# Performance work log

Measured on AMD Instinct MI355X. Metric: run time of the kernel, lower is better.

The kernel has to match this reference:

```python
import jax, jax.numpy as jnp
import numpy as np

T = 0.07        # temperature (hardcoded in CCM)
BN_EPS = 1e-5   # torch BatchNorm1d default eps (eval mode, running stats)


def _l2norm(x):
    # torch F.normalize(dim=1): x / max(||x||, 1e-12)
    n = jnp.linalg.norm(x, axis=1, keepdims=True)
    return x / jnp.maximum(n, 1e-12)


def _attn(q, k):
    # cosine similarity scaled by 1/t and 1/sqrt(num_keys)
    scale = jnp.asarray(k.shape[0], q.dtype) ** 0.5
    return (_l2norm(q) @ _l2norm(k).T) / T / scale


def setup_inputs() -> dict:
    key = jax.random.key(0)
    ks = jax.random.split(key, 24)
    D, N, BS, C, H = 2048, 1024, 64, 65, 128
    f32 = jnp.float32
    def g(k, shape, scale=1.0):
        return jax.random.normal(k, shape, f32) * scale
    return {
        "all_f": g(ks[0], (BS, D)),
        "embedding": _l2norm(g(ks[1], (N, D))),  # memory queue (normalized at init)
        "all_y": jax.random.randint(ks[2], (BS,), 0, C),
        "head_w1": g(ks[3], (D, H), 1.0 / np.sqrt(D)),
        "head_b1": jnp.zeros((H,), f32),
        "head_g": jax.random.uniform(ks[4], (H,), f32) + 0.5,
        "head_beta": g(ks[5], (H,), 0.1),
        "head_rm": g(ks[6], (H,), 0.1),
        "head_rv": jax.random.uniform(ks[7], (H,), f32) + 0.5,
        "head_w2": g(ks[8], (H, H), 1.0 / np.sqrt(H)),
        "head_b2": jnp.zeros((H,), f32),
        "mix_w1": g(ks[9], (2 * H, H), 1.0 / np.sqrt(2 * H)),
        "mix_b1": jnp.zeros((H,), f32),
        "mix_g": jax.random.uniform(ks[10], (H,), f32) + 0.5,
        "mix_beta": g(ks[11], (H,), 0.1),
        "mix_rm": g(ks[12], (H,), 0.1),
        "mix_rv": jax.random.uniform(ks[13], (H,), f32) + 0.5,
        "mix_w2": g(ks[14], (H, D), 1.0 / np.sqrt(H)),
        "mix_b2": jnp.zeros((D,), f32),
        "clf_w": g(ks[15], (D, C), 1.0 / np.sqrt(D)),
        "clf_b": jnp.zeros((C,), f32),
    }


def reference(all_f, embedding, all_y,
              head_w1, head_b1, head_g, head_beta, head_rm, head_rv, head_w2, head_b2,
              mix_w1, mix_b1, mix_g, mix_beta, mix_rm, mix_rv, mix_w2, mix_b2,
              clf_w, clf_b):
    # CCM.causal(all_f, embedding, all_y): returns [bs, num_classes]
    H = head_b2.shape[0]
    # z|x attention over the memory queue
    z_x = jax.nn.softmax(_attn(all_f, embedding), axis=-1)          # [bs, N]

    def head(x):
        h = x @ head_w1 + head_b1
        h = (h - head_rm) * jax.lax.rsqrt(head_rv + BN_EPS) * head_g + head_beta
        return jax.nn.relu(h) @ head_w2 + head_b2                   # [., 128]

    hf = head(all_f)        # [bs, 128]
    hz = head(embedding)    # [N, 128]
    # mixer layer 1 on concat([hf, hz]) decomposed into two matmuls + broadcast add
    h1 = hf @ mix_w1[:H] + mix_b1                                   # [bs, 128]
    h1 = h1[:, None, :] + (hz @ mix_w1[H:])[None, :, :]             # [bs, N, 128]
    h1 = (h1 - mix_rm) * jax.lax.rsqrt(mix_rv + BN_EPS) * mix_g + mix_beta
    h1 = jax.nn.relu(h1)
    mixed = h1 @ mix_w2 + mix_b2                                    # [bs, N, D]
    y_zx = jax.nn.softmax(mixed @ clf_w + clf_b, axis=-1)           # [bs, N, C] = p(y|z,x)
    # p(x): self-attention row-sums, softmax over the batch (all_y given -> this branch)
    p_x = jax.nn.softmax(_attn(all_f, all_f).sum(axis=1), axis=0)   # [bs]
    sum_x = jnp.einsum('b,bnc->nc', p_x, y_zx)                      # [N, C]
    return z_x @ sum_x                                              # [bs, C]
```

## Files before the change

### kernel.cpp

```cpp
#include <hip/hip_runtime.h>
#include <hip/hip_bf16.h>
#include <math.h>

#define D   2048
#define NQ  1024
#define BSZ 64
#define NC  65
#define HD  128

#define OFF_SCALEH 0
#define OFF_CH     128
#define OFF_BZC    256
#define OFF_BAC    384
#define OFF_BVEC   512
#define OFF_PXP    640
#define OFF_WC     896
#define OFF_A2T    6016
#define OFF_B2     14208
#define OFF_SP     145280
#define OFF_SUMX   669568
#define OFF_FNB    751488
#define OFF_AFB    817024
#define OFF_EMBB   882560
#define OFF_W1T    1931136
#define OFF_WZT    2062208
#define OFF_WAT    2070400
#define OFF_MW2B   2078592
#define OFF_CWT    2226048

typedef __attribute__((ext_vector_type(8))) short    bf16x8;
typedef __attribute__((ext_vector_type(4))) float    f32x4;
typedef __attribute__((ext_vector_type(8))) unsigned short u16x8;
typedef __attribute__((ext_vector_type(2))) unsigned short u16x2;

__device__ inline unsigned short f2b(float v) {
    __hip_bfloat16 h = __float2bfloat16(v);
    return __builtin_bit_cast(unsigned short, h);
}

__global__ void __launch_bounds__(256) k_prep(const float* __restrict__ all_f,
                                              const float* __restrict__ emb,
                                              const float* __restrict__ head_w1,
                                              const float* __restrict__ head_b1,
                                              const float* __restrict__ head_g,
                                              const float* __restrict__ head_beta,
                                              const float* __restrict__ head_rm,
                                              const float* __restrict__ head_rv,
                                              const float* __restrict__ head_w2,
                                              const float* __restrict__ head_b2,
                                              const float* __restrict__ mix_w1,
                                              const float* __restrict__ mix_b1,
                                              const float* __restrict__ mix_g,
                                              const float* __restrict__ mix_beta,
                                              const float* __restrict__ mix_rm,
                                              const float* __restrict__ mix_rv,
                                              const float* __restrict__ mix_w2,
                                              const float* __restrict__ mix_b2,
                                              const float* __restrict__ clf_w,
                                              float* __restrict__ ws) {
    __shared__ float sbuf[128*66];
    int bid = blockIdx.x, t = threadIdx.x;
    if (bid == 0) {
        int h = t & 127, jq = t >> 7;
        float sb = 0.f, sa = 0.f;
        #pragma unroll 8
        for (int j = jq*64; j < jq*64 + 64; ++j) {
            float b2v = head_b2[j];
            sb = fmaf(b2v, mix_w1[(HD + j)*HD + h], sb);
            sa = fmaf(b2v, mix_w1[j*HD + h], sa);
        }
        sbuf[jq*256 + h]       = sb;
        sbuf[jq*256 + 128 + h] = sa;
        __syncthreads();
        if (jq == 0) {
            float s = head_g[h] * rsqrtf(head_rv[h] + 1e-5f);
            ws[OFF_SCALEH + h] = s;
            ws[OFF_CH + h] = (head_b1[h] - head_rm[h]) * s + head_beta[h];
            float ms = mix_g[h] * rsqrtf(mix_rv[h] + 1e-5f);
            float msh = mix_beta[h] - mix_rm[h] * ms;
            float sbT = sbuf[h] + sbuf[256 + h];
            float saT = sbuf[128 + h] + sbuf[256 + 128 + h];
            ws[OFF_BZC + h] = sbT * ms;
            ws[OFF_BAC + h] = fmaf(saT + mix_b1[h], ms, msh);
        }
    } else if (bid < 129) {
        int j = bid - 1;
        int h = t & 127, which = t >> 7;
        const float* M1 = mix_w1 + (which ? 0 : HD*HD);
        float ms = mix_g[h] * rsqrtf(mix_rv[h] + 1e-5f);
        float acc = 0.f;
        #pragma unroll 8
        for (int k = 0; k < HD; ++k)
            acc = fmaf(head_w2[j*HD + k], M1[k*HD + h], acc);
        unsigned short* dst = (unsigned short*)(ws + (which ? OFF_WAT : OFF_WZT));
        dst[h*HD + j] = f2b(acc * ms);
    } else if (bid < 147) {
        int r0 = (bid - 129) * 8;
        unsigned short* dst = (unsigned short*)(ws + OFF_MW2B);
        int i0 = t * 8;
        for (int rr = 0; rr < 8; ++rr) {
            int r = r0 + rr;
            u16x8 o;
            if (r < HD || r == HD) {
                const float* src = (r < HD) ? (mix_w2 + (size_t)r * D) : mix_b2;
                float4 f1 = *(const float4*)(src + i0);
                float4 f2 = *(const float4*)(src + i0 + 4);
                o[0]=f2b(f1.x); o[1]=f2b(f1.y); o[2]=f2b(f1.z); o[3]=f2b(f1.w);
                o[4]=f2b(f2.x); o[5]=f2b(f2.y); o[6]=f2b(f2.z); o[7]=f2b(f2.w);
            } else {
                o[0]=0;o[1]=0;o[2]=0;o[3]=0;o[4]=0;o[5]=0;o[6]=0;o[7]=0;
            }
            *(u16x8*)(dst + (size_t)r*D + i0) = o;
        }
    } else if (bid < 163) {
        int k0 = (bid - 147) * 128;
        float (*tile)[66] = (float(*)[66])sbuf;
        for (int i = t; i < 128*65; i += 256) {
            int r = i / 65;
            tile[r][i - 65*r] = clf_w[(size_t)k0*65 + i];
        }
        __syncthreads();
        unsigned short* cwt = (unsigned short*)(ws + OFF_CWT);
        for (int idx = t; idx < 80*16; idx += 256) {
            int c = idx >> 4, kq = idx & 15;
            u16x8 v;
            #pragma unroll
            for (int j = 0; j < 8; ++j)
                v[j] = (c < NC) ? f2b(tile[kq*8 + j][c]) : (unsigned short)0;
            *(u16x8*)(cwt + (size_t)c*D + k0 + kq*8) = v;
        }
    } else if (bid < 227) {
        int b = bid - 163;
        const float* src = all_f + (size_t)b * D;
        int i0 = t * 8;
        float4 f1 = *(const float4*)(src + i0);
        float4 f2 = *(const float4*)(src + i0 + 4);
        float s = f1.x*f1.x + f1.y*f1.y + f1.z*f1.z + f1.w*f1.w
                + f2.x*f2.x + f2.y*f2.y + f2.z*f2.z + f2.w*f2.w;
        sbuf[t] = s; __syncthreads();
        for (int k = 128; k > 0; k >>= 1) { if (t < k) sbuf[t] += sbuf[t + k]; __syncthreads(); }
        float rn = 1.f / fmaxf(sqrtf(sbuf[0]), 1e-12f);
        unsigned short* fnb = (unsigned short*)(ws + OFF_FNB) + (size_t)b * D;
        unsigned short* afb = (unsigned short*)(ws + OFF_AFB) + (size_t)b * D;
        u16x8 on, oa;
        on[0]=f2b(f1.x*rn); on[1]=f2b(f1.y*rn); on[2]=f2b(f1.z*rn); on[3]=f2b(f1.w*rn);
        on[4]=f2b(f2.x*rn); on[5]=f2b(f2.y*rn); on[6]=f2b(f2.z*rn); on[7]=f2b(f2.w*rn);
        oa[0]=f2b(f1.x); oa[1]=f2b(f1.y); oa[2]=f2b(f1.z); oa[3]=f2b(f1.w);
        oa[4]=f2b(f2.x); oa[5]=f2b(f2.y); oa[6]=f2b(f2.z); oa[7]=f2b(f2.w);
        *(u16x8*)(fnb + i0) = on;
        *(u16x8*)(afb + i0) = oa;
    } else if (bid < 483) {
        int n0 = (bid - 227) * 4;
        unsigned short* dst = (unsigned short*)(ws + OFF_EMBB);
        int i0 = t * 8;
        for (int r = 0; r < 4; ++r) {
            const float* src = emb + (size_t)(n0 + r) * D;
            float4 f1 = *(const float4*)(src + i0);
            float4 f2 = *(const float4*)(src + i0 + 4);
            u16x8 o;
            o[0]=f2b(f1.x); o[1]=f2b(f1.y); o[2]=f2b(f1.z); o[3]=f2b(f1.w);
            o[4]=f2b(f2.x); o[5]=f2b(f2.y); o[6]=f2b(f2.z); o[7]=f2b(f2.w);
            *(u16x8*)(dst + (size_t)(n0 + r)*D + i0) = o;
        }
    } else {
        int rb = bid - 483;
        float (*tile)[33] = (float(*)[33])sbuf;
        int k0 = (rb >> 2) * 128, h0 = (rb & 3) * 32;
        int hh = t & 31, kk = t >> 5;
        for (int r = 0; r < 16; ++r)
            tile[kk + r*8][hh] = head_w1[(size_t)(k0 + kk + r*8)*HD + h0 + hh];
        __syncthreads();
        unsigned short* dst = (unsigned short*)(ws + OFF_W1T);
        int kcol = (t & 63) * 2, hrow = t >> 6;
        for (int r = 0; r < 8; ++r) {
            int h = hrow + r*4;
            u16x2 v;
            v[0] = f2b(tile[kcol][h]);
            v[1] = f2b(tile[kcol + 1][h]);
            *(u16x2*)(dst + (size_t)(h0 + h)*D + k0 + kcol) = v;
        }
    }
}

__global__ void __launch_bounds__(512) k_main(const float* __restrict__ clf_b,
                                              float* __restrict__ ws) {
    __shared__ float part[2][32][128];
    __shared__ unsigned short ush[32][136];
    __shared__ float wcp[8][16][16];
    int bid = blockIdx.x, t = threadIdx.x;
    int lane = t & 63, wv = t >> 6;
    int row16 = lane & 15, kgrp = lane >> 4;
    if (bid < 128) {
        const unsigned short* fnb  = (const unsigned short*)(ws + OFF_FNB);
        const unsigned short* embb = (const unsigned short*)(ws + OFF_EMBB);
        int nt = bid & 15, ks = bid >> 4;
        int b0 = (wv & 3) * 16;
        int n0 = nt*64 + (wv >> 2) * 32;
        const unsigned short* Ap = fnb  + (size_t)(b0 + row16)*D + ks*256 + kgrp*8;
        const unsigned short* B0 = embb + (size_t)(n0 + row16)*D + ks*256 + kgrp*8;
        const unsigned short* B1 = B0 + 16*D;
        f32x4 a0 = {0,0,0,0}, a1 = {0,0,0,0};
        #pragma unroll
        for (int s = 0; s < 8; ++s) {
            bf16x8 a = *(const bf16x8*)(Ap + s*32);
            a0 = __builtin_amdgcn_mfma_f32_16x16x32_bf16(a, *(const bf16x8*)(B0 + s*32), a0, 0, 0, 0);
            a1 = __builtin_amdgcn_mfma_f32_16x16x32_bf16(a, *(const bf16x8*)(B1 + s*32), a1, 0, 0, 0);
        }
        float* Sp = ws + OFF_SP + (size_t)ks * BSZ * NQ;
        #pragma unroll
        for (int r = 0; r < 4; ++r) {
            float* rowp = Sp + (size_t)(b0 + kgrp*4 + r)*NQ + n0;
            rowp[row16]      = a0[r];
            rowp[16 + row16] = a1[r];
        }
    } else if (bid < 162) {
        int tile = bid - 128;
        bool isF = tile >= 32;
        const unsigned short* Arow = isF
            ? (const unsigned short*)(ws + OFF_AFB) + (size_t)(tile - 32) * 32 * D
            : (const unsigned short*)(ws + OFF_EMBB) + (size_t)tile * 32 * D;
        const unsigned short* w1t = (const unsigned short*)(ws + OFF_W1T);
        int hgrp = wv & 3, kh = wv >> 2;
        const unsigned short* Ap = Arow + (size_t)row16*D + kh*1024 + kgrp*8;
        const unsigned short* B0 = w1t + (size_t)(hgrp*32 + row16)*D + kh*1024 + kgrp*8;
        const unsigned short* B1 = B0 + 16*D;
        f32x4 h00 = {0,0,0,0}, h01 = {0,0,0,0}, h10 = {0,0,0,0}, h11 = {0,0,0,0};
        #pragma unroll 4
        for (int s = 0; s < 32; ++s) {
            bf16x8 a0 = *(const bf16x8*)(Ap + s*32);
            bf16x8 a1 = *(const bf16x8*)(Ap + 16*D + s*32);
            bf16x8 b0 = *(const bf16x8*)(B0 + s*32);
            bf16x8 b1 = *(const bf16x8*)(B1 + s*32);
            h00 = __builtin_amdgcn_mfma_f32_16x16x32_bf16(a0, b0, h00, 0, 0, 0);
            h01 = __builtin_amdgcn_mfma_f32_16x16x32_bf16(a0, b1, h01, 0, 0, 0);
            h10 = __builtin_amdgcn_mfma_f32_16x16x32_bf16(a1, b0, h10, 0, 0, 0);
            h11 = __builtin_amdgcn_mfma_f32_16x16x32_bf16(a1, b1, h11, 0, 0, 0);
        }
        int mb = kgrp*4, hc0 = hgrp*32 + row16, hc1 = hc0 + 16;
        #pragma unroll
        for (int r = 0; r < 4; ++r) {
            part[kh][mb + r][hc0]      = h00[r];
            part[kh][mb + r][hc1]      = h01[r];
            part[kh][16 + mb + r][hc0] = h10[r];
            part[kh][16 + mb + r][hc1] = h11[r];
        }
        __syncthreads();
        {
            int row = t >> 4, cg = (t & 15) * 8;
            #pragma unroll
            for (int j = 0; j < 8; ++j) {
                int col = cg + j;
                float v = part[0][row][col] + part[1][row][col];
                ush[row][col] = f2b(fmaxf(fmaf(v, ws[OFF_SCALEH + col], ws[OFF_CH + col]), 0.f));
            }
        }
        __syncthreads();
        {
            int rt = wv >> 2, wv2 = wv & 3;
            const unsigned short* wt = (const unsigned short*)(ws + (isF ? OFF_WAT : OFF_WZT));
            const unsigned short* W0 = wt + (size_t)(wv2*32 + row16)*HD + kgrp*8;
            const unsigned short* W1b = W0 + 16*HD;
            f32x4 o0 = {0,0,0,0}, o1 = {0,0,0,0};
            #pragma unroll
            for (int s = 0; s < 4; ++s) {
                bf16x8 a = *(const bf16x8*)(&ush[rt*16 + row16][s*32 + kgrp*8]);
                o0 = __builtin_amdgcn_mfma_f32_16x16x32_bf16(a, *(const bf16x8*)(W0 + s*32), o0, 0, 0, 0);
                o1 = __builtin_amdgcn_mfma_f32_16x16x32_bf16(a, *(const bf16x8*)(W1b + s*32), o1, 0, 0, 0);
            }
            int hcA = wv2*32 + row16, hcB = hcA + 16;
            int boff = isF ? OFF_BAC : OFF_BZC;
            float bz0 = ws[boff + hcA], bz1 = ws[boff + hcB];
            float* outp = isF ? (ws + OFF_A2T + (size_t)(tile - 32)*32*HD)
                              : (ws + OFF_B2  + (size_t)tile*32*HD);
            #pragma unroll
            for (int r = 0; r < 4; ++r) {
                outp[(size_t)(rt*16 + mb + r)*HD + hcA] = o0[r] + bz0;
                outp[(size_t)(rt*16 + mb + r)*HD + hcB] = o1[r] + bz1;
            }
        }
    } else if (bid < 207) {
        int w = bid - 162;
        int mt = w / 5, ntile = w % 5;
        const unsigned short* mw2b = (const unsigned short*)(ws + OFF_MW2B);
        const unsigned short* cwt  = (const unsigned short*)(ws + OFF_CWT);
        const unsigned short* Ap = mw2b + (size_t)(mt*16 + row16)*D + wv*256 + kgrp*8;
        const unsigned short* Bp = cwt  + (size_t)(ntile*16 + row16)*D + wv*256 + kgrp*8;
        f32x4 acc = {0,0,0,0};
        #pragma unroll
        for (int s = 0; s < 8; ++s)
            acc = __builtin_amdgcn_mfma_f32_16x16x32_bf16(
                *(const bf16x8*)(Ap + s*32), *(const bf16x8*)(Bp + s*32), acc, 0, 0, 0);
        #pragma unroll
        for (int r = 0; r < 4; ++r)
            wcp[wv][kgrp*4 + r][row16] = acc[r];
        __syncthreads();
        if (t < 256) {
            int j = t >> 4, c16 = t & 15;
            float s = 0.f;
            #pragma unroll
            for (int q = 0; q < 8; ++q) s += wcp[q][j][c16];
            int jj = mt*16 + j, c = ntile*16 + c16;
            unsigned short* wct = (unsigned short*)(ws + OFF_WC);
            if (jj < HD)       wct[(size_t)c*HD + jj] = f2b(s);
            else if (jj == HD) ws[OFF_BVEC + c] = (c < NC) ? s + clf_b[c] : -1e30f;
        }
    } else {
        int pb = bid - 207;
        const unsigned short* fnb = (const unsigned short*)(ws + OFF_FNB);
        int bq = wv & 3, kq = (wv >> 2) + pb*2;
        int b0 = bq*16;
        const unsigned short* Ap = fnb + (size_t)(b0 + row16)*D + kq*512 + kgrp*8;
        const unsigned short* Bp = fnb + (size_t)row16*D + kq*512 + kgrp*8;
        f32x4 acc[4];
        #pragma unroll
        for (int nt = 0; nt < 4; ++nt) acc[nt] = (f32x4){0.f,0.f,0.f,0.f};
        #pragma unroll 2
        for (int s = 0; s < 16; ++s) {
            bf16x8 a = *(const bf16x8*)(Ap + s*32);
            #pragma unroll
            for (int nt = 0; nt < 4; ++nt)
                acc[nt] = __builtin_amdgcn_mfma_f32_16x16x32_bf16(
                    a, *(const bf16x8*)(Bp + (size_t)nt*16*D + s*32), acc[nt], 0, 0, 0);
        }
        #pragma unroll
        for (int r = 0; r < 4; ++r) {
            float v = acc[0][r] + acc[1][r] + acc[2][r] + acc[3][r];
            v += __shfl_xor(v, 1); v += __shfl_xor(v, 2);
            v += __shfl_xor(v, 4); v += __shfl_xor(v, 8);
            if (row16 == 0)
                ws[OFF_PXP + kq*64 + b0 + kgrp*4 + r] = v;
        }
    }
}

__global__ void __launch_bounds__(256) k_mix_mfma(float* __restrict__ ws) {
    __shared__ unsigned short wcs[80][136];
    __shared__ float redp[4][80];
    int t = threadIdx.x, lane = t & 63, wv = t >> 6;
    int n = blockIdx.x;
    int row16 = lane & 15, kgrp = lane >> 4;
    const unsigned short* wct = (const unsigned short*)(ws + OFF_WC);
    for (int i = t; i < 80*16; i += 256) {
        int r = i >> 4, cc = (i & 15) * 8;
        *(u16x8*)&wcs[r][cc] = *(const u16x8*)(wct + (size_t)r*HD + cc);
    }
    const float invTS = 1.0f / (0.07f * 8.0f);
    float sv = (ws[OFF_PXP + lane] + ws[OFF_PXP + 64 + lane]
              + ws[OFF_PXP + 128 + lane] + ws[OFF_PXP + 192 + lane]) * invTS;
    float m2 = sv;
    m2 = fmaxf(m2, __shfl_xor(m2, 1));  m2 = fmaxf(m2, __shfl_xor(m2, 2));
    m2 = fmaxf(m2, __shfl_xor(m2, 4));  m2 = fmaxf(m2, __shfl_xor(m2, 8));
    m2 = fmaxf(m2, __shfl_xor(m2, 16)); m2 = fmaxf(m2, __shfl_xor(m2, 32));
    float e2 = __expf(sv - m2);
    float su = e2;
    su += __shfl_xor(su, 1);  su += __shfl_xor(su, 2);  su += __shfl_xor(su, 4);
    su += __shfl_xor(su, 8);  su += __shfl_xor(su, 16); su += __shfl_xor(su, 32);
    float px = e2 / su;

    float bvl[5];
    #pragma unroll
    for (int ct = 0; ct < 5; ++ct) bvl[ct] = ws[OFF_BVEC + ct*16 + row16];
    __syncthreads();

    const float* b2r = ws + OFF_B2 + (size_t)n * HD;
    const float* a2r = ws + OFF_A2T + (size_t)(wv*16 + row16) * HD;
    bf16x8 af[4];
    #pragma unroll
    for (int kt = 0; kt < 4; ++kt) {
        const float* ap = a2r + kt*32 + kgrp*8;
        const float* bp = b2r + kt*32 + kgrp*8;
        float4 alo = *(const float4*)(ap);
        float4 ahi = *(const float4*)(ap + 4);
        float4 blo = *(const float4*)(bp);
        float4 bhi = *(const float4*)(bp + 4);
        bf16x8 v;
        v[0] = (short)f2b(fmaxf(alo.x + blo.x, 0.f));
        v[1] = (short)f2b(fmaxf(alo.y + blo.y, 0.f));
        v[2] = (short)f2b(fmaxf(alo.z + blo.z, 0.f));
        v[3] = (short)f2b(fmaxf(alo.w + blo.w, 0.f));
        v[4] = (short)f2b(fmaxf(ahi.x + bhi.x, 0.f));
        v[5] = (short)f2b(fmaxf(ahi.y + bhi.y, 0.f));
        v[6] = (short)f2b(fmaxf(ahi.z + bhi.z, 0.f));
        v[7] = (short)f2b(fmaxf(ahi.w + bhi.w, 0.f));
        af[kt] = v;
    }
    f32x4 acc[5];
    #pragma unroll
    for (int ct = 0; ct < 5; ++ct) acc[ct] = (f32x4){0.f,0.f,0.f,0.f};
    #pragma unroll
    for (int ct = 0; ct < 5; ++ct)
        #pragma unroll
        for (int kt = 0; kt < 4; ++kt)
            acc[ct] = __builtin_amdgcn_mfma_f32_16x16x32_bf16(
                af[kt], *(const bf16x8*)(&wcs[ct*16 + row16][kt*32 + kgrp*8]), acc[ct], 0, 0, 0);

    float outp[5] = {0.f, 0.f, 0.f, 0.f, 0.f};
    #pragma unroll
    for (int r = 0; r < 4; ++r) {
        float v0 = acc[0][r] + bvl[0];
        float v1 = acc[1][r] + bvl[1];
        float v2 = acc[2][r] + bvl[2];
        float v3 = acc[3][r] + bvl[3];
        float v4 = acc[4][r] + bvl[4];
        float m = fmaxf(fmaxf(fmaxf(v0, v1), fmaxf(v2, v3)), v4);
        m = fmaxf(m, __shfl_xor(m, 1)); m = fmaxf(m, __shfl_xor(m, 2));
        m = fmaxf(m, __shfl_xor(m, 4)); m = fmaxf(m, __shfl_xor(m, 8));
        float e0 = __expf(v0 - m), e1 = __expf(v1 - m), e2v = __expf(v2 - m);
        float e3 = __expf(v3 - m), e4 = __expf(v4 - m);
        float s = e0 + e1 + e2v + e3 + e4;
        s += __shfl_xor(s, 1); s += __shfl_xor(s, 2);
        s += __shfl_xor(s, 4); s += __shfl_xor(s, 8);
        float pxr = __shfl(px, wv*16 + kgrp*4 + r);
        float scale = pxr / s;
        outp[0] = fmaf(e0, scale, outp[0]);
        outp[1] = fmaf(e1, scale, outp[1]);
        outp[2] = fmaf(e2v, scale, outp[2]);
        outp[3] = fmaf(e3, scale, outp[3]);
        outp[4] = fmaf(e4, scale, outp[4]);
    }
    #pragma unroll
    for (int ct = 0; ct < 5; ++ct) {
        float v = outp[ct];
        v += __shfl_xor(v, 16); v += __shfl_xor(v, 32);
        outp[ct] = v;
    }
    if (kgrp == 0) {
        #pragma unroll
        for (int ct = 0; ct < 5; ++ct) redp[wv][ct*16 + row16] = outp[ct];
    }
    __syncthreads();
    if (t < 80) {
        ws[OFF_SUMX + (size_t)n*80 + t] = redp[0][t] + redp[1][t] + redp[2][t] + redp[3][t];
    }
}

__global__ void __launch_bounds__(512) k_outz(const float* __restrict__ ws, float* __restrict__ out) {
    __shared__ float red8m[8], red8s[8];
    __shared__ float zrow[NQ];
    __shared__ float parts[8][128];
    int b = blockIdx.x, t = threadIdx.x;
    int lane = t & 63, wvv = t >> 6;
    const float invTS = 1.0f / (0.07f * 32.0f);
    const float* Sp = ws + OFF_SP + (size_t)b * NQ;
    float v0, v1;
    {
        float s = 0.f;
        #pragma unroll
        for (int p = 0; p < 8; ++p) s += Sp[(size_t)p*BSZ*NQ + t];
        v0 = s * invTS;
        s = 0.f;
        #pragma unroll
        for (int p = 0; p < 8; ++p) s += Sp[(size_t)p*BSZ*NQ + 512 + t];
        v1 = s * invTS;
    }
    float vmax = fmaxf(v0, v1);
    vmax = fmaxf(vmax, __shfl_xor(vmax, 1));  vmax = fmaxf(vmax, __shfl_xor(vmax, 2));
    vmax = fmaxf(vmax, __shfl_xor(vmax, 4));  vmax = fmaxf(vmax, __shfl_xor(vmax, 8));
    vmax = fmaxf(vmax, __shfl_xor(vmax, 16)); vmax = fmaxf(vmax, __shfl_xor(vmax, 32));
    if (lane == 0) red8m[wvv] = vmax;
    __syncthreads();
    float m = red8m[0];
    #pragma unroll
    for (int q = 1; q < 8; ++q) m = fmaxf(m, red8m[q]);
    float e0 = __expf(v0 - m), e1 = __expf(v1 - m);
    float ss = e0 + e1;
    ss += __shfl_xor(ss, 1);  ss += __shfl_xor(ss, 2);  ss += __shfl_xor(ss, 4);
    ss += __shfl_xor(ss, 8);  ss += __shfl_xor(ss, 16); ss += __shfl_xor(ss, 32);
    if (lane == 0) red8s[wvv] = ss;
    __syncthreads();
    float S = red8s[0] + red8s[1] + red8s[2] + red8s[3]
            + red8s[4] + red8s[5] + red8s[6] + red8s[7];
    float inv = 1.f / S;
    zrow[t]       = e0 * inv;
    zrow[512 + t] = e1 * inv;
    __syncthreads();
    const float* Sx = ws + OFF_SUMX;
    int c2 = 64 + (lane & 15);
    int nbase = wvv * 128;
    float a0 = 0.f, a1 = 0.f;
    #pragma unroll 8
    for (int k = 0; k < 128; ++k) {
        float z = zrow[nbase + k];
        const float* srow = Sx + (size_t)(nbase + k) * 80;
        a0 = fmaf(z, srow[lane], a0);
        a1 = fmaf(z, srow[c2], a1);
    }
    parts[wvv][lane] = a0;
    if (lane < 16) parts[wvv][64 + lane] = a1;
    __syncthreads();
    if (t < NC) {
        float s = 0.f;
        #pragma unroll
        for (int q = 0; q < 8; ++q) s += parts[q][t];
        out[b*NC + t] = s;
    }
}

extern "C" void kernel_launch(void* const* d_in, const int* in_sizes, int n_in,
                              void* d_out, int out_size, void* d_ws, size_t ws_size,
                              hipStream_t stream) {
    const float* all_f    = (const float*)d_in[0];
    const float* emb      = (const float*)d_in[1];
    const float* head_w1  = (const float*)d_in[3];
    const float* head_b1  = (const float*)d_in[4];
    const float* head_g   = (const float*)d_in[5];
    const float* head_beta= (const float*)d_in[6];
    const float* head_rm  = (const float*)d_in[7];
    const float* head_rv  = (const float*)d_in[8];
    const float* head_w2  = (const float*)d_in[9];
    const float* head_b2  = (const float*)d_in[10];
    const float* mix_w1   = (const float*)d_in[11];
    const float* mix_b1   = (const float*)d_in[12];
    const float* mix_g    = (const float*)d_in[13];
    const float* mix_beta = (const float*)d_in[14];
    const float* mix_rm   = (const float*)d_in[15];
    const float* mix_rv   = (const float*)d_in[16];
    const float* mix_w2   = (const float*)d_in[17];
    const float* mix_b2   = (const float*)d_in[18];
    const float* clf_w    = (const float*)d_in[19];
    const float* clf_b    = (const float*)d_in[20];
    float* ws  = (float*)d_ws;
    float* out = (float*)d_out;

    hipLaunchKernelGGL(k_prep, dim3(547), dim3(256), 0, stream,
                       all_f, emb, head_w1, head_b1, head_g, head_beta, head_rm, head_rv,
                       head_w2, head_b2, mix_w1, mix_b1, mix_g, mix_beta, mix_rm, mix_rv,
                       mix_w2, mix_b2, clf_w, ws);
    hipLaunchKernelGGL(k_main,     dim3(209),  dim3(512), 0, stream, clf_b, ws);
    hipLaunchKernelGGL(k_mix_mfma, dim3(1024), dim3(256), 0, stream, ws);
    hipLaunchKernelGGL(k_outz,     dim3(64),   dim3(512), 0, stream, ws, out);
}
```

Before: 65.67 us.

## Fuse main, mix and output kernels into one cooperative kernel with grid syncs

Replaces the three kernels that followed k_prep with a single cooperative kernel of 256 blocks that uses grid.sync between phases. The head-layer GEMM is split over twice as many blocks, with partial sums staged through a new global buffer and finished in a later phase. The mix phase now handles four queue rows per block with A2 cached in shared memory, and shared memory is reused across phases through a union. The aim is to remove launch overhead and raise parallelism in the head GEMM, at the cost of grid-wide barriers, an extra global round trip for the partials, and fewer, larger blocks in the mix phase.

```diff
diff --git a/kernel.cpp b/kernel.cpp
--- a/kernel.cpp
+++ b/kernel.cpp
@@ -1,6 +1,9 @@
 #include <hip/hip_runtime.h>
+#include <hip/hip_cooperative_groups.h>
 #include <hip/hip_bf16.h>
 #include <math.h>
+
+namespace cg = cooperative_groups;
 
 #define D   2048
 #define NQ  1024
@@ -27,6 +30,7 @@
 #define OFF_WAT    2070400
 #define OFF_MW2B   2078592
 #define OFF_CWT    2226048
+#define OFF_H1P    2307968
 
 typedef __attribute__((ext_vector_type(8))) short    bf16x8;
 typedef __attribute__((ext_vector_type(4))) float    f32x4;
@@ -182,14 +186,21 @@
     }
 }
 
-__global__ void __launch_bounds__(512) k_main(const float* __restrict__ clf_b,
-                                              float* __restrict__ ws) {
-    __shared__ float part[2][32][128];
-    __shared__ unsigned short ush[32][136];
-    __shared__ float wcp[8][16][16];
+__global__ void __launch_bounds__(512, 2) k_fused(const float* __restrict__ clf_b,
+                                                  float* __restrict__ ws,
+                                                  float* __restrict__ out) {
+    cg::grid_group grid = cg::this_grid();
+    union SU {
+        struct { float part[2][32][128]; float wcp[8][16][16]; } p1;
+        struct { unsigned short ush[32][136]; } p15;
+        struct { unsigned short wcs[80][136]; float a2s[64][132]; float redp[8][80]; } p2;
+        struct { float red8m[8]; float red8s[8]; float zrow[NQ]; float parts[8][128]; } p3;
+    };
+    __shared__ SU su;
     int bid = blockIdx.x, t = threadIdx.x;
     int lane = t & 63, wv = t >> 6;
     int row16 = lane & 15, kgrp = lane >> 4;
+
     if (bid < 128) {
         const unsigned short* fnb  = (const unsigned short*)(ws + OFF_FNB);
         const unsigned short* embb = (const unsigned short*)(ws + OFF_EMBB);
@@ -213,20 +224,22 @@
             rowp[row16]      = a0[r];
             rowp[16 + row16] = a1[r];
         }
-    } else if (bid < 162) {
-        int tile = bid - 128;
+    } else if (bid < 196) {
+        int role = bid - 128;
+        int tile = role >> 1, kh = role & 1;
         bool isF = tile >= 32;
         const unsigned short* Arow = isF
             ? (const unsigned short*)(ws + OFF_AFB) + (size_t)(tile - 32) * 32 * D
             : (const unsigned short*)(ws + OFF_EMBB) + (size_t)tile * 32 * D;
         const unsigned short* w1t = (const unsigned short*)(ws + OFF_W1T);
-        int hgrp = wv & 3, kh = wv >> 2;
-        const unsigned short* Ap = Arow + (size_t)row16*D + kh*1024 + kgrp*8;
-        const unsigned short* B0 = w1t + (size_t)(hgrp*32 + row16)*D + kh*1024 + kgrp*8;
+        int hgrp = wv & 3, kq = wv >> 2;
+        int koff = kh*1024 + kq*512;
+        const unsigned short* Ap = Arow + (size_t)row16*D + koff + kgrp*8;
+        const unsigned short* B0 = w1t + (size_t)(hgrp*32 + row16)*D + koff + kgrp*8;
         const unsigned short* B1 = B0 + 16*D;
         f32x4 h00 = {0,0,0,0}, h01 = {0,0,0,0}, h10 = {0,0,0,0}, h11 = {0,0,0,0};
         #pragma unroll 4
-        for (int s = 0; s < 32; ++s) {
+        for (int s = 0; s < 16; ++s) {
             bf16x8 a0 = *(const bf16x8*)(Ap + s*32);
             bf16x8 a1 = *(const bf16x8*)(Ap + 16*D + s*32);
             bf16x8 b0 = *(const bf16x8*)(B0 + s*32);
@@ -239,47 +252,27 @@
         int mb = kgrp*4, hc0 = hgrp*32 + row16, hc1 = hc0 + 16;
         #pragma unroll
         for (int r = 0; r < 4; ++r) {
-            part[kh][mb + r][hc0]      = h00[r];
-            part[kh][mb + r][hc1]      = h01[r];
-            part[kh][16 + mb + r][hc0] = h10[r];
-            part[kh][16 + mb + r][hc1] = h11[r];
-        }
-        __syncthreads();
-        {
-            int row = t >> 4, cg = (t & 15) * 8;
-            #pragma unroll
-            for (int j = 0; j < 8; ++j) {
-                int col = cg + j;
-                float v = part[0][row][col] + part[1][row][col];
-                ush[row][col] = f2b(fmaxf(fmaf(v, ws[OFF_SCALEH + col], ws[OFF_CH + col]), 0.f));
-            }
-        }
-        __syncthreads();
-        {
-            int rt = wv >> 2, wv2 = wv & 3;
-            const unsigned short* wt = (const unsigned short*)(ws + (isF ? OFF_WAT : OFF_WZT));
-            const unsigned short* W0 = wt + (size_t)(wv2*32 + row16)*HD + kgrp*8;
-            const unsigned short* W1b = W0 + 16*HD;
-            f32x4 o0 = {0,0,0,0}, o1 = {0,0,0,0};
-            #pragma unroll
-            for (int s = 0; s < 4; ++s) {
-                bf16x8 a = *(const bf16x8*)(&ush[rt*16 + row16][s*32 + kgrp*8]);
-                o0 = __builtin_amdgcn_mfma_f32_16x16x32_bf16(a, *(const bf16x8*)(W0 + s*32), o0, 0, 0, 0);
-                o1 = __builtin_amdgcn_mfma_f32_16x16x32_bf16(a, *(const bf16x8*)(W1b + s*32), o1, 0, 0, 0);
-            }
-            int hcA = wv2*32 + row16, hcB = hcA + 16;
-            int boff = isF ? OFF_BAC : OFF_BZC;
-            float bz0 = ws[boff + hcA], bz1 = ws[boff + hcB];
-            float* outp = isF ? (ws + OFF_A2T + (size_t)(tile - 32)*32*HD)
-                              : (ws + OFF_B2  + (size_t)tile*32*HD);
-            #pragma unroll
-            for (int r = 0; r < 4; ++r) {
-                outp[(size_t)(rt*16 + mb + r)*HD + hcA] = o0[r] + bz0;
-                outp[(size_t)(rt*16 + mb + r)*HD + hcB] = o1[r] + bz1;
-            }
-        }
-    } else if (bid < 207) {
-        int w = bid - 162;
+            su.p1.part[kq][mb + r][hc0]      = h00[r];
+            su.p1.part[kq][mb + r][hc1]      = h01[r];
+            su.p1.part[kq][16 + mb + r][hc0] = h10[r];
+            su.p1.part[kq][16 + mb + r][hc1] = h11[r];
+        }
+        __syncthreads();
+        int row = t >> 4, c8 = (t & 15) * 8;
+        float* dst = ws + OFF_H1P + (size_t)kh*1088*HD + (size_t)(tile*32 + row)*HD + c8;
+        float4 o0, o1;
+        o0.x = su.p1.part[0][row][c8+0] + su.p1.part[1][row][c8+0];
+        o0.y = su.p1.part[0][row][c8+1] + su.p1.part[1][row][c8+1];
+        o0.z = su.p1.part[0][row][c8+2] + su.p1.part[1][row][c8+2];
+        o0.w = su.p1.part[0][row][c8+3] + su.p1.part[1][row][c8+3];
+        o1.x = su.p1.part[0][row][c8+4] + su.p1.part[1][row][c8+4];
+        o1.y = su.p1.part[0][row][c8+5] + su.p1.part[1][row][c8+5];
+        o1.z = su.p1.part[0][row][c8+6] + su.p1.part[1][row][c8+6];
+        o1.w = su.p1.part[0][row][c8+7] + su.p1.part[1][row][c8+7];
+        *(float4*)dst = o0;
+        *(float4*)(dst + 4) = o1;
+    } else if (bid < 241) {
+        int w = bid - 196;
         int mt = w / 5, ntile = w % 5;
         const unsigned short* mw2b = (const unsigned short*)(ws + OFF_MW2B);
         const unsigned short* cwt  = (const unsigned short*)(ws + OFF_CWT);
@@ -292,20 +285,20 @@
                 *(const bf16x8*)(Ap + s*32), *(const bf16x8*)(Bp + s*32), acc, 0, 0, 0);
         #pragma unroll
         for (int r = 0; r < 4; ++r)
-            wcp[wv][kgrp*4 + r][row16] = acc[r];
+            su.p1.wcp[wv][kgrp*4 + r][row16] = acc[r];
         __syncthreads();
         if (t < 256) {
             int j = t >> 4, c16 = t & 15;
             float s = 0.f;
             #pragma unroll
-            for (int q = 0; q < 8; ++q) s += wcp[q][j][c16];
+            for (int q = 0; q < 8; ++q) s += su.p1.wcp[q][j][c16];
             int jj = mt*16 + j, c = ntile*16 + c16;
             unsigned short* wct = (unsigned short*)(ws + OFF_WC);
             if (jj < HD)       wct[(size_t)c*HD + jj] = f2b(s);
             else if (jj == HD) ws[OFF_BVEC + c] = (c < NC) ? s + clf_b[c] : -1e30f;
         }
-    } else {
-        int pb = bid - 207;
+    } else if (bid < 243) {
+        int pb = bid - 241;
         const unsigned short* fnb = (const unsigned short*)(ws + OFF_FNB);
         int bq = wv & 3, kq = (wv >> 2) + pb*2;
         int b0 = bq*16;
@@ -331,168 +324,212 @@
                 ws[OFF_PXP + kq*64 + b0 + kgrp*4 + r] = v;
         }
     }
-}
-
-__global__ void __launch_bounds__(256) k_mix_mfma(float* __restrict__ ws) {
-    __shared__ unsigned short wcs[80][136];
-    __shared__ float redp[4][80];
-    int t = threadIdx.x, lane = t & 63, wv = t >> 6;
-    int n = blockIdx.x;
-    int row16 = lane & 15, kgrp = lane >> 4;
-    const unsigned short* wct = (const unsigned short*)(ws + OFF_WC);
-    for (int i = t; i < 80*16; i += 256) {
-        int r = i >> 4, cc = (i & 15) * 8;
-        *(u16x8*)&wcs[r][cc] = *(const u16x8*)(wct + (size_t)r*HD + cc);
+    grid.sync();
+
+    if (bid < 34) {
+        int tile = bid;
+        bool isF = tile >= 32;
+        int row = t >> 4, c8 = (t & 15) * 8;
+        const float* h0p = ws + OFF_H1P + (size_t)(tile*32 + row)*HD + c8;
+        const float* h1p = h0p + (size_t)1088*HD;
+        #pragma unroll
+        for (int j = 0; j < 8; ++j) {
+            int col = c8 + j;
+            float v = h0p[j] + h1p[j];
+            su.p15.ush[row][col] = f2b(fmaxf(fmaf(v, ws[OFF_SCALEH + col], ws[OFF_CH + col]), 0.f));
+        }
+        __syncthreads();
+        int rt = wv >> 2, wv2 = wv & 3;
+        const unsigned short* wt = (const unsigned short*)(ws + (isF ? OFF_WAT : OFF_WZT));
+        const unsigned short* W0 = wt + (size_t)(wv2*32 + row16)*HD + kgrp*8;
+        const unsigned short* W1b = W0 + 16*HD;
+        f32x4 o0 = {0,0,0,0}, o1 = {0,0,0,0};
+        #pragma unroll
+        for (int s = 0; s < 4; ++s) {
+            bf16x8 a = *(const bf16x8*)(&su.p15.ush[rt*16 + row16][s*32 + kgrp*8]);
+            o0 = __builtin_amdgcn_mfma_f32_16x16x32_bf16(a, *(const bf16x8*)(W0 + s*32), o0, 0, 0, 0);
+            o1 = __builtin_amdgcn_mfma_f32_16x16x32_bf16(a, *(const bf16x8*)(W1b + s*32), o1, 0, 0, 0);
+        }
+        int hcA = wv2*32 + row16, hcB = hcA + 16;
+        int boff = isF ? OFF_BAC : OFF_BZC;
+        float bz0 = ws[boff + hcA], bz1 = ws[boff + hcB];
+        float* outp = isF ? (ws + OFF_A2T + (size_t)(tile - 32)*32*HD)
+                          : (ws + OFF_B2  + (size_t)tile*32*HD);
+        int mb = kgrp*4;
+        #pragma unroll
+        for (int r = 0; r < 4; ++r) {
+            outp[(size_t)(rt*16 + mb + r)*HD + hcA] = o0[r] + bz0;
+            outp[(size_t)(rt*16 + mb + r)*HD + hcB] = o1[r] + bz1;
+        }
     }
-    const float invTS = 1.0f / (0.07f * 8.0f);
-    float sv = (ws[OFF_PXP + lane] + ws[OFF_PXP + 64 + lane]
-              + ws[OFF_PXP + 128 + lane] + ws[OFF_PXP + 192 + lane]) * invTS;
-    float m2 = sv;
-    m2 = fmaxf(m2, __shfl_xor(m2, 1));  m2 = fmaxf(m2, __shfl_xor(m2, 2));
-    m2 = fmaxf(m2, __shfl_xor(m2, 4));  m2 = fmaxf(m2, __shfl_xor(m2, 8));
-    m2 = fmaxf(m2, __shfl_xor(m2, 16)); m2 = fmaxf(m2, __shfl_xor(m2, 32));
-    float e2 = __expf(sv - m2);
-    float su = e2;
-    su += __shfl_xor(su, 1);  su += __shfl_xor(su, 2);  su += __shfl_xor(su, 4);
-    su += __shfl_xor(su, 8);  su += __shfl_xor(su, 16); su += __shfl_xor(su, 32);
-    float px = e2 / su;
-
-    float bvl[5];
-    #pragma unroll
-    for (int ct = 0; ct < 5; ++ct) bvl[ct] = ws[OFF_BVEC + ct*16 + row16];
-    __syncthreads();
-
-    const float* b2r = ws + OFF_B2 + (size_t)n * HD;
-    const float* a2r = ws + OFF_A2T + (size_t)(wv*16 + row16) * HD;
-    bf16x8 af[4];
-    #pragma unroll
-    for (int kt = 0; kt < 4; ++kt) {
-        const float* ap = a2r + kt*32 + kgrp*8;
-        const float* bp = b2r + kt*32 + kgrp*8;
-        float4 alo = *(const float4*)(ap);
-        float4 ahi = *(const float4*)(ap + 4);
-        float4 blo = *(const float4*)(bp);
-        float4 bhi = *(const float4*)(bp + 4);
-        bf16x8 v;
-        v[0] = (short)f2b(fmaxf(alo.x + blo.x, 0.f));
-        v[1] = (short)f2b(fmaxf(alo.y + blo.y, 0.f));
-        v[2] = (short)f2b(fmaxf(alo.z + blo.z, 0.f));
-        v[3] = (short)f2b(fmaxf(alo.w + blo.w, 0.f));
-        v[4] = (short)f2b(fmaxf(ahi.x + bhi.x, 0.f));
-        v[5] = (short)f2b(fmaxf(ahi.y + bhi.y, 0.f));
-        v[6] = (short)f2b(fmaxf(ahi.z + bhi.z, 0.f));
-        v[7] = (short)f2b(fmaxf(ahi.w + bhi.w, 0.f));
-        af[kt] = v;
+    grid.sync();
+
+    {
+        const unsigned short* wct = (const unsigned short*)(ws + OFF_WC);
+        for (int i = t; i < 80*16; i += 512) {
+            int r = i >> 4, cc = (i & 15) * 8;
+            *(u16x8*)&su.p2.wcs[r][cc] = *(const u16x8*)(wct + (size_t)r*HD + cc);
+        }
+        const float* a2g = ws + OFF_A2T;
+        for (int i = t; i < 64*32; i += 512) {
+            int r = i >> 5, q = i & 31;
+            *(float4*)&su.p2.a2s[r][q*4] = *(const float4*)(a2g + (size_t)r*HD + q*4);
+        }
+        const float invTS = 1.0f / (0.07f * 8.0f);
+        float sv = (ws[OFF_PXP + lane] + ws[OFF_PXP + 64 + lane]
+                  + ws[OFF_PXP + 128 + lane] + ws[OFF_PXP + 192 + lane]) * invTS;
+        float m2 = sv;
+        m2 = fmaxf(m2, __shfl_xor(m2, 1));  m2 = fmaxf(m2, __shfl_xor(m2, 2));
+        m2 = fmaxf(m2, __shfl_xor(m2, 4));  m2 = fmaxf(m2, __shfl_xor(m2, 8));
+        m2 = fmaxf(m2, __shfl_xor(m2, 16)); m2 = fmaxf(m2, __shfl_xor(m2, 32));
+        float e2 = __expf(sv - m2);
+        float ssum = e2;
+        ssum += __shfl_xor(ssum, 1);  ssum += __shfl_xor(ssum, 2);  ssum += __shfl_xor(ssum, 4);
+        ssum += __shfl_xor(ssum, 8);  ssum += __shfl_xor(ssum, 16); ssum += __shfl_xor(ssum, 32);
+        float px = e2 / ssum;
+        float bvl[5];
+        #pragma unroll
+        for (int ct = 0; ct < 5; ++ct) bvl[ct] = ws[OFF_BVEC + ct*16 + row16];
+        __syncthreads();
+        int bt = wv & 3, ng = wv >> 2;
+        #pragma unroll
+        for (int it = 0; it < 2; ++it) {
+            int n = bid*4 + it*2 + ng;
+            const float* b2r = ws + OFF_B2 + (size_t)n * HD;
+            bf16x8 af[4];
+            #pragma unroll
+            for (int kt = 0; kt < 4; ++kt) {
+                const float* ap = &su.p2.a2s[bt*16 + row16][kt*32 + kgrp*8];
+                float4 alo = *(const float4*)(ap);
+                float4 ahi = *(const float4*)(ap + 4);
+                float4 blo = *(const float4*)(b2r + kt*32 + kgrp*8);
+                float4 bhi = *(const float4*)(b2r + kt*32 + kgrp*8 + 4);
+                bf16x8 v;
+                v[0] = (short)f2b(fmaxf(alo.x + blo.x, 0.f));
+                v[1] = (short)f2b(fmaxf(alo.y + blo.y, 0.f));
+                v[2] = (short)f2b(fmaxf(alo.z + blo.z, 0.f));
+                v[3] = (short)f2b(fmaxf(alo.w + blo.w, 0.f));
+                v[4] = (short)f2b(fmaxf(ahi.x + bhi.x, 0.f));
+                v[5] = (short)f2b(fmaxf(ahi.y + bhi.y, 0.f));
+                v[6] = (short)f2b(fmaxf(ahi.z + bhi.z, 0.f));
+                v[7] = (short)f2b(fmaxf(ahi.w + bhi.w, 0.f));
+                af[kt] = v;
+            }
+            f32x4 acc[5];
+            #pragma unroll
+            for (int ct = 0; ct < 5; ++ct) acc[ct] = (f32x4){0.f,0.f,0.f,0.f};
+            #pragma unroll
+            for (int ct = 0; ct < 5; ++ct)
+                #pragma unroll
+                for (int kt = 0; kt < 4; ++kt)
+                    acc[ct] = __builtin_amdgcn_mfma_f32_16x16x32_bf16(
+                        af[kt], *(const bf16x8*)(&su.p2.wcs[ct*16 + row16][kt*32 + kgrp*8]),
+                        acc[ct], 0, 0, 0);
+            float outp[5] = {0.f, 0.f, 0.f, 0.f, 0.f};
+            #pragma unroll
+            for (int r = 0; r < 4; ++r) {
+                float v0 = acc[0][r] + bvl[0];
+                float v1 = acc[1][r] + bvl[1];
+                float v2 = acc[2][r] + bvl[2];
+                float v3 = acc[3][r] + bvl[3];
+                float v4 = acc[4][r] + bvl[4];
+                float m = fmaxf(fmaxf(fmaxf(v0, v1), fmaxf(v2, v3)), v4);
+                m = fmaxf(m, __shfl_xor(m, 1)); m = fmaxf(m, __shfl_xor(m, 2));
+                m = fmaxf(m, __shfl_xor(m, 4)); m = fmaxf(m, __shfl_xor(m, 8));
+                float e0 = __expf(v0 - m), e1 = __expf(v1 - m), e2v = __expf(v2 - m);
+                float e3 = __expf(v3 - m), e4 = __expf(v4 - m);
+                float s = e0 + e1 + e2v + e3 + e4;
+                s += __shfl_xor(s, 1); s += __shfl_xor(s, 2);
+                s += __shfl_xor(s, 4); s += __shfl_xor(s, 8);
+                float pxr = __shfl(px, bt*16 + kgrp*4 + r);
+                float scale = pxr / s;
+                outp[0] = fmaf(e0, scale, outp[0]);
+                outp[1] = fmaf(e1, scale, outp[1]);
+                outp[2] = fmaf(e2v, scale, outp[2]);
+                outp[3] = fmaf(e3, scale, outp[3]);
+                outp[4] = fmaf(e4, scale, outp[4]);
+            }
+            #pragma unroll
+            for (int ct = 0; ct < 5; ++ct) {
+                float v = outp[ct];
+                v += __shfl_xor(v, 16); v += __shfl_xor(v, 32);
+                outp[ct] = v;
+            }
+            if (kgrp == 0) {
+                #pragma unroll
+                for (int ct = 0; ct < 5; ++ct) su.p2.redp[wv][ct*16 + row16] = outp[ct];
+            }
+            __syncthreads();
+            if (t < 160) {
+                int half = (t >= 80) ? 1 : 0;
+                int c = t - 80*half;
+                int nn = bid*4 + it*2 + half;
+                ws[OFF_SUMX + (size_t)nn*80 + c] =
+                    su.p2.redp[half*4 + 0][c] + su.p2.redp[half*4 + 1][c]
+                  + su.p2.redp[half*4 + 2][c] + su.p2.redp[half*4 + 3][c];
+            }
+            __syncthreads();
+        }
     }
-    f32x4 acc[5];
-    #pragma unroll
-    for (int ct = 0; ct < 5; ++ct) acc[ct] = (f32x4){0.f,0.f,0.f,0.f};
-    #pragma unroll
-    for (int ct = 0; ct < 5; ++ct)
-        #pragma unroll
-        for (int kt = 0; kt < 4; ++kt)
-            acc[ct] = __builtin_amdgcn_mfma_f32_16x16x32_bf16(
-                af[kt], *(const bf16x8*)(&wcs[ct*16 + row16][kt*32 + kgrp*8]), acc[ct], 0, 0, 0);
-
-    float outp[5] = {0.f, 0.f, 0.f, 0.f, 0.f};
-    #pragma unroll
-    for (int r = 0; r < 4; ++r) {
-        float v0 = acc[0][r] + bvl[0];
-        float v1 = acc[1][r] + bvl[1];
-        float v2 = acc[2][r] + bvl[2];
-        float v3 = acc[3][r] + bvl[3];
-        float v4 = acc[4][r] + bvl[4];
-        float m = fmaxf(fmaxf(fmaxf(v0, v1), fmaxf(v2, v3)), v4);
-        m = fmaxf(m, __shfl_xor(m, 1)); m = fmaxf(m, __shfl_xor(m, 2));
-        m = fmaxf(m, __shfl_xor(m, 4)); m = fmaxf(m, __shfl_xor(m, 8));
-        float e0 = __expf(v0 - m), e1 = __expf(v1 - m), e2v = __expf(v2 - m);
-        float e3 = __expf(v3 - m), e4 = __expf(v4 - m);
-        float s = e0 + e1 + e2v + e3 + e4;
-        s += __shfl_xor(s, 1); s += __shfl_xor(s, 2);
-        s += __shfl_xor(s, 4); s += __shfl_xor(s, 8);
-        float pxr = __shfl(px, wv*16 + kgrp*4 + r);
-        float scale = pxr / s;
-        outp[0] = fmaf(e0, scale, outp[0]);
-        outp[1] = fmaf(e1, scale, outp[1]);
-        outp[2] = fmaf(e2v, scale, outp[2]);
-        outp[3] = fmaf(e3, scale, outp[3]);
-        outp[4] = fmaf(e4, scale, outp[4]);
-    }
-    #pragma unroll
-    for (int ct = 0; ct < 5; ++ct) {
-        float v = outp[ct];
-        v += __shfl_xor(v, 16); v += __shfl_xor(v, 32);
-        outp[ct] = v;
-    }
-    if (kgrp == 0) {
-        #pragma unroll
-        for (int ct = 0; ct < 5; ++ct) redp[wv][ct*16 + row16] = outp[ct];
-    }
-    __syncthreads();
-    if (t < 80) {
-        ws[OFF_SUMX + (size_t)n*80 + t] = redp[0][t] + redp[1][t] + redp[2][t] + redp[3][t];
-    }
-}
-
-__global__ void __launch_bounds__(512) k_outz(const float* __restrict__ ws, float* __restrict__ out) {
-    __shared__ float red8m[8], red8s[8];
-    __shared__ float zrow[NQ];
-    __shared__ float parts[8][128];
-    int b = blockIdx.x, t = threadIdx.x;
-    int lane = t & 63, wvv = t >> 6;
-    const float invTS = 1.0f / (0.07f * 32.0f);
-    const float* Sp = ws + OFF_SP + (size_t)b * NQ;
-    float v0, v1;
+    grid.sync();
+
+    if (bid >= 64) return;
     {
-        float s = 0.f;
-        #pragma unroll
-        for (int p = 0; p < 8; ++p) s += Sp[(size_t)p*BSZ*NQ + t];
-        v0 = s * invTS;
-        s = 0.f;
-        #pragma unroll
-        for (int p = 0; p < 8; ++p) s += Sp[(size_t)p*BSZ*NQ + 512 + t];
-        v1 = s * invTS;
-    }
-    float vmax = fmaxf(v0, v1);
-    vmax = fmaxf(vmax, __shfl_xor(vmax, 1));  vmax = fmaxf(vmax, __shfl_xor(vmax, 2));
-    vmax = fmaxf(vmax, __shfl_xor(vmax, 4));  vmax = fmaxf(vmax, __shfl_xor(vmax, 8));
-    vmax = fmaxf(vmax, __shfl_xor(vmax, 16)); vmax = fmaxf(vmax, __shfl_xor(vmax, 32));
-    if (lane == 0) red8m[wvv] = vmax;
-    __syncthreads();
-    float m = red8m[0];
-    #pragma unroll
-    for (int q = 1; q < 8; ++q) m = fmaxf(m, red8m[q]);
-    float e0 = __expf(v0 - m), e1 = __expf(v1 - m);
-    float ss = e0 + e1;
-    ss += __shfl_xor(ss, 1);  ss += __shfl_xor(ss, 2);  ss += __shfl_xor(ss, 4);
-    ss += __shfl_xor(ss, 8);  ss += __shfl_xor(ss, 16); ss += __shfl_xor(ss, 32);
-    if (lane == 0) red8s[wvv] = ss;
-    __syncthreads();
-    float S = red8s[0] + red8s[1] + red8s[2] + red8s[3]
-            + red8s[4] + red8s[5] + red8s[6] + red8s[7];
-    float inv = 1.f / S;
-    zrow[t]       = e0 * inv;
-    zrow[512 + t] = e1 * inv;
-    __syncthreads();
-    const float* Sx = ws + OFF_SUMX;
-    int c2 = 64 + (lane & 15);
-    int nbase = wvv * 128;
-    float a0 = 0.f, a1 = 0.f;
-    #pragma unroll 8
-    for (int k = 0; k < 128; ++k) {
-        float z = zrow[nbase + k];
-        const float* srow = Sx + (size_t)(nbase + k) * 80;
-        a0 = fmaf(z, srow[lane], a0);
-        a1 = fmaf(z, srow[c2], a1);
-    }
-    parts[wvv][lane] = a0;
-    if (lane < 16) parts[wvv][64 + lane] = a1;
-    __syncthreads();
-    if (t < NC) {
-        float s = 0.f;
-        #pragma unroll
-        for (int q = 0; q < 8; ++q) s += parts[q][t];
-        out[b*NC + t] = s;
+        int b = bid;
+        const float invTS = 1.0f / (0.07f * 32.0f);
+        const float* Sp = ws + OFF_SP + (size_t)b * NQ;
+        float v0, v1;
+        {
+            float s = 0.f;
+            #pragma unroll
+            for (int p = 0; p < 8; ++p) s += Sp[(size_t)p*BSZ*NQ + t];
+            v0 = s * invTS;
+            s = 0.f;
+            #pragma unroll
+            for (int p = 0; p < 8; ++p) s += Sp[(size_t)p*BSZ*NQ + 512 + t];
+            v1 = s * invTS;
+        }
+        float vmax = fmaxf(v0, v1);
+        vmax = fmaxf(vmax, __shfl_xor(vmax, 1));  vmax = fmaxf(vmax, __shfl_xor(vmax, 2));
+        vmax = fmaxf(vmax, __shfl_xor(vmax, 4));  vmax = fmaxf(vmax, __shfl_xor(vmax, 8));
+        vmax = fmaxf(vmax, __shfl_xor(vmax, 16)); vmax = fmaxf(vmax, __shfl_xor(vmax, 32));
+        if (lane == 0) su.p3.red8m[wv] = vmax;
+        __syncthreads();
+        float m = su.p3.red8m[0];
+        #pragma unroll
+        for (int q = 1; q < 8; ++q) m = fmaxf(m, su.p3.red8m[q]);
+        float e0 = __expf(v0 - m), e1 = __expf(v1 - m);
+        float ss = e0 + e1;
+        ss += __shfl_xor(ss, 1);  ss += __shfl_xor(ss, 2);  ss += __shfl_xor(ss, 4);
+        ss += __shfl_xor(ss, 8);  ss += __shfl_xor(ss, 16); ss += __shfl_xor(ss, 32);
+        if (lane == 0) su.p3.red8s[wv] = ss;
+        __syncthreads();
+        float S = su.p3.red8s[0] + su.p3.red8s[1] + su.p3.red8s[2] + su.p3.red8s[3]
+                + su.p3.red8s[4] + su.p3.red8s[5] + su.p3.red8s[6] + su.p3.red8s[7];
+        float inv = 1.f / S;
+        su.p3.zrow[t]       = e0 * inv;
+        su.p3.zrow[512 + t] = e1 * inv;
+        __syncthreads();
+        const float* Sx = ws + OFF_SUMX;
+        int c2 = 64 + (lane & 15);
+        int nbase = wv * 128;
+        float a0 = 0.f, a1 = 0.f;
+        #pragma unroll 8
+        for (int k = 0; k < 128; ++k) {
+            float z = su.p3.zrow[nbase + k];
+            const float* srow = Sx + (size_t)(nbase + k) * 80;
+            a0 = fmaf(z, srow[lane], a0);
+            a1 = fmaf(z, srow[c2], a1);
+        }
+        su.p3.parts[wv][lane] = a0;
+        if (lane < 16) su.p3.parts[wv][64 + lane] = a1;
+        __syncthreads();
+        if (t < NC) {
+            float s = 0.f;
+            #pragma unroll
+            for (int q = 0; q < 8; ++q) s += su.p3.parts[q][t];
+            out[b*NC + t] = s;
+        }
     }
 }
 
@@ -526,7 +563,9 @@
                        all_f, emb, head_w1, head_b1, head_g, head_beta, head_rm, head_rv,
                        head_w2, head_b2, mix_w1, mix_b1, mix_g, mix_beta, mix_rm, mix_rv,
                        mix_w2, mix_b2, clf_w, ws);
-    hipLaunchKernelGGL(k_main,     dim3(209),  dim3(512), 0, stream, clf_b, ws);
-    hipLaunchKernelGGL(k_mix_mfma, dim3(1024), dim3(256), 0, stream, ws);
-    hipLaunchKernelGGL(k_outz,     dim3(64),   dim3(512), 0, stream, ws, out);
+    void* kargs[3];
+    kargs[0] = (void*)&clf_b;
+    kargs[1] = (void*)&ws;
+    kargs[2] = (void*)&out;
+    hipLaunchCooperativeKernel((void*)k_fused, dim3(256), dim3(512), kargs, 0, stream);
 }
```

New measurement: 153.9 us. +134.4%, slower.
